# Kernel optimization log

Hardware: AMD Instinct MI355X
Metric: run time of the kernel (lower is better)

The kernel has to match this reference:

```python
import jax, jax.numpy as jnp
import numpy as np

IN_DIM, OUT_DIM, N_PROTO, RANK = 1024, 1024, 32, 16


def setup_inputs() -> dict:
    key = jax.random.key(0)
    ks = jax.random.split(key, 5)
    x = jax.random.normal(ks[0], (2, 4096, IN_DIM), dtype=jnp.float32)
    prototypes = jax.random.normal(ks[1], (N_PROTO, IN_DIM), dtype=jnp.float32) * 0.02
    B = jax.random.normal(ks[2], (N_PROTO, RANK, IN_DIM), dtype=jnp.float32) * 0.02
    A = jax.random.normal(ks[3], (N_PROTO, OUT_DIM, RANK), dtype=jnp.float32) * 0.02
    bias = jnp.zeros((N_PROTO, OUT_DIM), dtype=jnp.float32)
    temp = jnp.asarray(1.0, dtype=jnp.float32)
    return {"x": x, "prototypes": prototypes, "B": B, "A": A, "bias": bias, "temp": temp}


def reference(x, prototypes, B, A, bias, temp):
    lead = x.shape[:-1]
    xf = x.reshape(-1, IN_DIM)                       # [N, in]
    x2 = jnp.sum(xf * xf, axis=1, keepdims=True)     # [N,1]
    p2 = jnp.sum(prototypes * prototypes, axis=1)    # [P]
    d2 = x2 + p2[None, :] - 2.0 * (xf @ prototypes.T)
    dists = jnp.sqrt(jnp.maximum(d2, 0.0))           # [N,P]
    t = jnp.maximum(jnp.abs(temp), 0.1)
    w = jax.nn.softmax(-dists / t, axis=1)           # [N,P]
    topw, topi = jax.lax.top_k(w, 2)                 # [N,2]
    topw = topw / jnp.sum(topw, axis=1, keepdims=True)
    out = jnp.zeros((xf.shape[0], OUT_DIM), dtype=xf.dtype)
    for tslot in range(2):
        idx = topi[:, tslot]                          # [N]
        wt = topw[:, tslot:tslot + 1]                 # [N,1]
        h = jnp.einsum('nri,ni->nr', B[idx], xf)      # gathered low-rank down-proj
        y = jnp.einsum('nor,nr->no', A[idx], h) + bias[idx]
        out = out + wt * y
    return out.reshape(*lead, OUT_DIM)
```

## Files before the change

### kernel.cpp

```cpp
#include <hip/hip_runtime.h>
#include <math.h>

#define ROWS_TOTAL 8192
#define KDIM 1024
#define NPROTO 32
#define RNK 16
#define OUTD 1024
#define TIE_EPS 1.30e-4
#define DELTA 4.0e-5f
#define FLAG_CAP 4096

__global__ __launch_bounds__(256) void prep_kernel(
    const float* __restrict__ A, const float* __restrict__ B,
    const float* __restrict__ proto, float* __restrict__ At,
    float* __restrict__ Bt, float* __restrict__ Pt, double* __restrict__ p2g,
    int* __restrict__ counts, int* __restrict__ flagcnt)
{
    __shared__ float T[16 * 68];
    __shared__ float U[64 * 20];
    __shared__ double red[32][9];
    __shared__ float TP[32][33];
    const int tid = threadIdx.x;

    if (blockIdx.x < 32) {
        const int p = blockIdx.x;
        const float4* B4 = (const float4*)(B + (size_t)p * RNK * KDIM);
        const float4* A4 = (const float4*)(A + (size_t)p * OUTD * RNK);
        float4* Bt4 = (float4*)(Bt + (size_t)p * KDIM * RNK);
        float4* At4 = (float4*)(At + (size_t)p * RNK * OUTD);
        for (int c = 0; c < 16; ++c) {
            {
                int r = tid >> 4, kk = tid & 15;
                float4 v = B4[r * 256 + c * 16 + kk];
                *(float4*)&T[r * 68 + kk * 4] = v;
            }
            {
                int o = tid >> 2, rq = tid & 3;
                float4 v = A4[(c * 64 + o) * 4 + rq];
                *(float4*)&U[o * 20 + rq * 4] = v;
            }
            __syncthreads();
            {
                int k = tid >> 2, rq = tid & 3;
                float4 g = make_float4(T[(rq * 4 + 0) * 68 + k], T[(rq * 4 + 1) * 68 + k],
                                       T[(rq * 4 + 2) * 68 + k], T[(rq * 4 + 3) * 68 + k]);
                Bt4[(c * 64 + k) * 4 + rq] = g;
            }
            {
                int r = tid >> 4, ow = tid & 15;
                float4 g = make_float4(U[(ow * 4 + 0) * 20 + r], U[(ow * 4 + 1) * 20 + r],
                                       U[(ow * 4 + 2) * 20 + r], U[(ow * 4 + 3) * 20 + r]);
                At4[r * 256 + c * 16 + ow] = g;
            }
            __syncthreads();
        }
    } else {
        if (tid < 64) counts[tid] = 0;
        if (tid == 64) flagcnt[0] = 0;
        {
            const int p = tid >> 3, seg = tid & 7;
            const float* a = proto + (size_t)p * KDIM + seg * 128;
            double s = 0.0;
            for (int k = 0; k < 128; ++k) {
                double v = (double)a[k];
                s = fma(v, v, s);
            }
            red[p][seg] = s;
        }
        __syncthreads();
        if (tid < 32) {
            double acc = red[tid][0];
            #pragma unroll
            for (int j = 1; j < 8; ++j) acc += red[tid][j];
            p2g[tid] = acc;
        }
        float4* Pt4 = (float4*)Pt;
        for (int kc = 0; kc < 32; ++kc) {
            {
                int cc = tid >> 3, kk4 = tid & 7;
                float4 v = *(const float4*)(proto + (size_t)cc * KDIM + kc * 32 + kk4 * 4);
                TP[cc][kk4 * 4 + 0] = v.x; TP[cc][kk4 * 4 + 1] = v.y;
                TP[cc][kk4 * 4 + 2] = v.z; TP[cc][kk4 * 4 + 3] = v.w;
            }
            __syncthreads();
            {
                int kk = tid >> 3, c4 = tid & 7;
                float4 g = make_float4(TP[c4 * 4 + 0][kk], TP[c4 * 4 + 1][kk],
                                       TP[c4 * 4 + 2][kk], TP[c4 * 4 + 3][kk]);
                Pt4[(kc * 32 + kk) * 8 + c4] = g;
            }
            __syncthreads();
        }
    }
}

#define INS(kb, ib) { \
    bool lt1 = (kb) < k1, lt2 = (kb) < k2, lt3 = (kb) < k3, lt4 = (kb) < k4; \
    float nk4 = lt3 ? k3 : (lt4 ? (kb) : k4); int ni4 = lt3 ? i3 : (lt4 ? (ib) : i4); \
    float nk3 = lt2 ? k2 : (lt3 ? (kb) : k3); int ni3 = lt2 ? i2 : (lt3 ? (ib) : i3); \
    float nk2 = lt1 ? k1 : (lt2 ? (kb) : k2); int ni2 = lt1 ? i1 : (lt2 ? (ib) : i2); \
    k4 = nk4; i4 = ni4; k3 = nk3; i3 = ni3; k2 = nk2; i2 = ni2; \
    if (lt1) { k1 = (kb); i1 = (ib); } }

__global__ __launch_bounds__(256) void route_kernel(
    const float* __restrict__ x, const float* __restrict__ Pt,
    const float* __restrict__ temp, const double* __restrict__ p2g,
    float4* __restrict__ route, int* __restrict__ counts,
    int* __restrict__ flagcnt, int* __restrict__ flaglist)
{
    __shared__ float Xs[8 * KDIM];
    __shared__ float part[4][8][33];
    __shared__ float x2p[4][8];
    __shared__ int lcnt[64];

    const int tid = threadIdx.x;
    const int w = tid >> 6, l = tid & 63;
    const int c4 = l & 7, kslot = l >> 3;
    const int rowbase = blockIdx.x * 8;

    if (tid < 64) lcnt[tid] = 0;

    const float4* x4 = (const float4*)x;
    float sq[8];
    #pragma unroll
    for (int j = 0; j < 8; ++j) {
        float4 v = x4[(size_t)rowbase * 256 + j * 256 + tid];
        ((float4*)Xs)[j * 256 + tid] = v;
        sq[j] = fmaf(v.x, v.x, fmaf(v.y, v.y, fmaf(v.z, v.z, v.w * v.w)));
    }
    #pragma unroll
    for (int m = 1; m < 64; m <<= 1) {
        #pragma unroll
        for (int j = 0; j < 8; ++j) sq[j] += __shfl_xor(sq[j], m);
    }
    if (l == 0) {
        #pragma unroll
        for (int j = 0; j < 8; ++j) x2p[w][j] = sq[j];
    }
    __syncthreads();

    float acc[8][4];
    #pragma unroll
    for (int j = 0; j < 8; ++j)
        #pragma unroll
        for (int jj = 0; jj < 4; ++jj) acc[j][jj] = 0.f;

    const float4* Pt4 = (const float4*)Pt;
    const int kbase = w * 256;
    #pragma unroll 4
    for (int i = 0; i < 32; ++i) {
        const int k = kbase + i * 8 + kslot;
        float4 pv = Pt4[k * 8 + c4];
        #pragma unroll
        for (int j = 0; j < 8; ++j) {
            float xv = Xs[j * KDIM + k];
            acc[j][0] = fmaf(xv, pv.x, acc[j][0]);
            acc[j][1] = fmaf(xv, pv.y, acc[j][1]);
            acc[j][2] = fmaf(xv, pv.z, acc[j][2]);
            acc[j][3] = fmaf(xv, pv.w, acc[j][3]);
        }
    }
    #pragma unroll
    for (int m = 8; m < 64; m <<= 1) {
        #pragma unroll
        for (int j = 0; j < 8; ++j) {
            acc[j][0] += __shfl_xor(acc[j][0], m);
            acc[j][1] += __shfl_xor(acc[j][1], m);
            acc[j][2] += __shfl_xor(acc[j][2], m);
            acc[j][3] += __shfl_xor(acc[j][3], m);
        }
    }
    if (kslot == 0) {
        #pragma unroll
        for (int j = 0; j < 8; ++j) {
            part[w][j][4 * c4 + 0] = acc[j][0];
            part[w][j][4 * c4 + 1] = acc[j][1];
            part[w][j][4 * c4 + 2] = acc[j][2];
            part[w][j][4 * c4 + 3] = acc[j][3];
        }
    }
    __syncthreads();

    {
        const int rowsel = tid >> 5, c = tid & 31;
        float dsum = (part[0][rowsel][c] + part[1][rowsel][c])
                   + (part[2][rowsel][c] + part[3][rowsel][c]);
        float key = (float)(p2g[c] - 2.0 * (double)dsum);
        float x2 = (x2p[0][rowsel] + x2p[1][rowsel])
                 + (x2p[2][rowsel] + x2p[3][rowsel]);

        float k1 = key, k2 = 3.0e38f, k3 = 3.1e38f, k4 = 3.2e38f;
        int i1 = c, i2 = 64, i3 = 65, i4 = 66;
        #pragma unroll
        for (int m = 1; m < 32; m <<= 1) {
            float b1 = __shfl_xor(k1, m), b2 = __shfl_xor(k2, m);
            float b3 = __shfl_xor(k3, m), b4 = __shfl_xor(k4, m);
            int j1 = __shfl_xor(i1, m), j2 = __shfl_xor(i2, m);
            int j3 = __shfl_xor(i3, m), j4 = __shfl_xor(i4, m);
            INS(b1, j1); INS(b2, j2); INS(b3, j3); INS(b4, j4);
        }
        if (c == 0) {
            const int row = rowbase + rowsel;
            const float tf = fmaxf(fabsf(temp[0]), 0.1f);
            bool amb = (k2 - k1 < DELTA) || (k3 - k2 < DELTA)
                    || (fabsf((k3 - k2) - (float)TIE_EPS) < DELTA)
                    || (k4 - k3 < DELTA);
            bool tie = (k3 - k2) < (float)TIE_EPS;
            bool take3 = tie && (i3 < i2);
            float ksel = take3 ? k3 : k2;
            int   isel = take3 ? i3 : i2;
            float d0 = sqrtf(fmaxf(x2 + k1, 0.f));
            float d1 = sqrtf(fmaxf(x2 + ksel, 0.f));
            float e = expf((d0 - d1) / tf);
            float w0 = 1.f / (1.f + e);
            route[row] = make_float4(__int_as_float(i1), __int_as_float(isel),
                                     w0, e * w0);
            atomicAdd(&lcnt[i1], 1);
            atomicAdd(&lcnt[32 + isel], 1);
            if (amb) {
                int fi = atomicAdd(flagcnt, 1);
                if (fi < FLAG_CAP) flaglist[fi] = row;
            }
        }
    }
    __syncthreads();
    if (tid < 64) atomicAdd(&counts[tid], lcnt[tid]);
}

__global__ __launch_bounds__(256) void refine_scan_kernel(
    const float* __restrict__ x, const float* __restrict__ proto,
    const float* __restrict__ temp, const double* __restrict__ p2g,
    float4* __restrict__ route, int* __restrict__ counts,
    const int* __restrict__ flagcnt, const int* __restrict__ flaglist,
    int2* __restrict__ segs)
{
    const int tid = threadIdx.x;
    const int w = tid >> 6, l = tid & 63;
    const int c = l & 31, half = l >> 5;
    const int n = min(flagcnt[0], FLAG_CAP);

    for (int f = w; f < n; f += 4) {
        const int row = flaglist[f];
        const float* xr = x + (size_t)row * KDIM;
        double xs = 0.0;
        for (int k = l * 16; k < l * 16 + 16; ++k) {
            double v = (double)xr[k];
            xs = fma(v, v, xs);
        }
        #pragma unroll
        for (int m = 1; m < 64; m <<= 1) xs += __shfl_xor(xs, m);
        const float* pr = proto + (size_t)c * KDIM + half * 512;
        const float* xh = xr + half * 512;
        double d0a = 0.0, d1a = 0.0;
        for (int k = 0; k < 512; k += 2) {
            d0a = fma((double)xh[k], (double)pr[k], d0a);
            d1a = fma((double)xh[k + 1], (double)pr[k + 1], d1a);
        }
        double acc = d0a + d1a;
        acc += __shfl_xor(acc, 32);
        double key = p2g[c] - 2.0 * acc;

        double k1 = key, k2 = 1.0e300, k3 = 1.1e300;
        int i1 = c, i2 = 64, i3 = 65;
        #pragma unroll
        for (int m = 1; m < 32; m <<= 1) {
            double b1 = __shfl_xor(k1, m), b2 = __shfl_xor(k2, m), b3 = __shfl_xor(k3, m);
            int j1 = __shfl_xor(i1, m), j2 = __shfl_xor(i2, m), j3 = __shfl_xor(i3, m);
            bool c1 = (k1 < b1) || (k1 == b1 && i1 < j1);
            double m1 = c1 ? k1 : b1, M1 = c1 ? b1 : k1;
            int mi1 = c1 ? i1 : j1, Mi1 = c1 ? j1 : i1;
            bool c2 = (k2 < b2) || (k2 == b2 && i2 < j2);
            double m2 = c2 ? k2 : b2;
            int mi2 = c2 ? i2 : j2;
            bool c3 = (k3 < b3) || (k3 == b3 && i3 < j3);
            double m3 = c3 ? k3 : b3;
            int mi3 = c3 ? i3 : j3;
            bool c4 = (M1 < m2) || (M1 == m2 && Mi1 < mi2);
            double t2 = c4 ? M1 : m2, T2 = c4 ? m2 : M1;
            int ti2 = c4 ? Mi1 : mi2, Ti2 = c4 ? mi2 : Mi1;
            bool c5 = (T2 < m3) || (T2 == m3 && Ti2 < mi3);
            k1 = m1; i1 = mi1;
            k2 = t2; i2 = ti2;
            k3 = c5 ? T2 : m3; i3 = c5 ? Ti2 : mi3;
        }
        if (l == 0) {
            const double tmp = (double)fmaxf(fabsf(temp[0]), 0.1f);
            bool tie = (k3 - k2) < TIE_EPS;
            bool take3 = tie && (i3 < i2);
            double ksel = take3 ? k3 : k2;
            int isel = take3 ? i3 : i2;
            double dd0 = sqrt(fmax(xs + k1, 0.0));
            double dd1 = sqrt(fmax(xs + ksel, 0.0));
            float e = expf((float)((dd0 - dd1) / tmp));
            float w0 = 1.f / (1.f + e);
            float4 old = route[row];
            int oi1 = __float_as_int(old.x), oisel = __float_as_int(old.y);
            if (oi1 != i1) { atomicAdd(&counts[oi1], -1); atomicAdd(&counts[i1], 1); }
            if (oisel != isel) { atomicAdd(&counts[32 + oisel], -1); atomicAdd(&counts[32 + isel], 1); }
            route[row] = make_float4(__int_as_float(i1), __int_as_float(isel),
                                     w0, e * w0);
        }
    }
    __syncthreads();
    if (tid < 64) {
        int v = atomicAdd(&counts[tid], 0);
        int sum = v;
        #pragma unroll
        for (int off = 1; off < 32; off <<= 1) {
            int u = __shfl_up(sum, off, 32);
            if ((tid & 31) >= off) sum += u;
        }
        counts[tid] = sum - v;
        segs[tid] = make_int2(sum - v, sum);
    }
}

__global__ __launch_bounds__(256) void scatter_kernel(
    const float4* __restrict__ route, int* __restrict__ counts,
    int* __restrict__ rowlist0, int* __restrict__ rowlist1)
{
    __shared__ int lcnt[64];
    __shared__ int gbase[64];
    const int tid = threadIdx.x;
    const int i = blockIdx.x * 256 + tid;
    if (tid < 64) lcnt[tid] = 0;
    __syncthreads();
    float4 rt = route[i];
    int p0 = __float_as_int(rt.x);
    int p1 = __float_as_int(rt.y);
    int lp0 = atomicAdd(&lcnt[p0], 1);
    int lp1 = atomicAdd(&lcnt[32 + p1], 1);
    __syncthreads();
    if (tid < 64) gbase[tid] = atomicAdd(&counts[tid], lcnt[tid]);
    __syncthreads();
    rowlist0[gbase[p0] + lp0] = i;
    rowlist1[gbase[32 + p1] + lp1] = i;
}

__global__ __launch_bounds__(256) void h_kernel(
    const float* __restrict__ x, const float* __restrict__ Bt,
    const int* __restrict__ rowlist0, const int* __restrict__ rowlist1,
    const int2* __restrict__ segs, float* __restrict__ hws)
{
    __shared__ float part[4][4][17];
    __shared__ int xoffs[4];

    const int tid = threadIdx.x;
    const int w = tid >> 6, l = tid & 63;
    const int kq = l >> 2, rq = l & 3;
    const int s = blockIdx.y;
    const int slot = s >> 5;
    const int2 sg = segs[s];
    const int* rl = slot ? rowlist1 : rowlist0;
    const float4* Btp = (const float4*)(Bt + (size_t)(s & 31) * KDIM * RNK);
    const int qbase = w * 256;

    for (int c = blockIdx.x; ; c += gridDim.x) {
        const int base = sg.x + c * 4;
        if (base >= sg.y) break;
        const int m = min(4, sg.y - base);

        if (tid < 4) xoffs[tid] = rl[base + min(tid, m - 1)] * KDIM;
        __syncthreads();
        const int x0 = xoffs[0], x1 = xoffs[1], x2 = xoffs[2], x3 = xoffs[3];

        float4 a0 = {0,0,0,0}, a1 = {0,0,0,0}, a2 = {0,0,0,0}, a3 = {0,0,0,0};
        #pragma unroll
        for (int i = 0; i < 16; ++i) {
            const int k = qbase + i * 16 + kq;
            float4 bv = Btp[k * 4 + rq];
            float v0 = x[x0 + k], v1 = x[x1 + k], v2 = x[x2 + k], v3 = x[x3 + k];
            a0.x = fmaf(v0, bv.x, a0.x); a0.y = fmaf(v0, bv.y, a0.y);
            a0.z = fmaf(v0, bv.z, a0.z); a0.w = fmaf(v0, bv.w, a0.w);
            a1.x = fmaf(v1, bv.x, a1.x); a1.y = fmaf(v1, bv.y, a1.y);
            a1.z = fmaf(v1, bv.z, a1.z); a1.w = fmaf(v1, bv.w, a1.w);
            a2.x = fmaf(v2, bv.x, a2.x); a2.y = fmaf(v2, bv.y, a2.y);
            a2.z = fmaf(v2, bv.z, a2.z); a2.w = fmaf(v2, bv.w, a2.w);
            a3.x = fmaf(v3, bv.x, a3.x); a3.y = fmaf(v3, bv.y, a3.y);
            a3.z = fmaf(v3, bv.z, a3.z); a3.w = fmaf(v3, bv.w, a3.w);
        }
        #pragma unroll
        for (int msk = 4; msk < 64; msk <<= 1) {
            a0.x += __shfl_xor(a0.x, msk); a0.y += __shfl_xor(a0.y, msk);
            a0.z += __shfl_xor(a0.z, msk); a0.w += __shfl_xor(a0.w, msk);
            a1.x += __shfl_xor(a1.x, msk); a1.y += __shfl_xor(a1.y, msk);
            a1.z += __shfl_xor(a1.z, msk); a1.w += __shfl_xor(a1.w, msk);
            a2.x += __shfl_xor(a2.x, msk); a2.y += __shfl_xor(a2.y, msk);
            a2.z += __shfl_xor(a2.z, msk); a2.w += __shfl_xor(a2.w, msk);
            a3.x += __shfl_xor(a3.x, msk); a3.y += __shfl_xor(a3.y, msk);
            a3.z += __shfl_xor(a3.z, msk); a3.w += __shfl_xor(a3.w, msk);
        }
        if (kq == 0) {
            *(float4*)&part[w][0][rq * 4] = a0;
            *(float4*)&part[w][1][rq * 4] = a1;
            *(float4*)&part[w][2][rq * 4] = a2;
            *(float4*)&part[w][3][rq * 4] = a3;
        }
        __syncthreads();
        if (tid < 64) {
            const int e = tid >> 4, r = tid & 15;
            if (e < m) {
                float hsum = part[0][e][r] + part[1][e][r]
                           + part[2][e][r] + part[3][e][r];
                hws[(size_t)(slot * ROWS_TOTAL + base + e) * 16 + r] = hsum;
            }
        }
        __syncthreads();
    }
}

__global__ __launch_bounds__(256) void y_kernel(
    const float* __restrict__ At, const float* __restrict__ bias,
    const float4* __restrict__ route, const int* __restrict__ rowlist,
    const int2* __restrict__ segs, const float* __restrict__ hws,
    float* __restrict__ out, int slot)
{
    __shared__ float hsm[16][17];
    __shared__ int rows[16];
    __shared__ float wts[16];

    const int tid = threadIdx.x;
    const int f4 = tid;
    const int p = blockIdx.y;
    const int2 sg = segs[slot * 32 + p];
    const float4* Atp = (const float4*)(At + (size_t)p * RNK * OUTD);
    const float4 bb = ((const float4*)(bias + (size_t)p * OUTD))[f4];

    float4 Areg[16];
    #pragma unroll
    for (int r = 0; r < 16; ++r) Areg[r] = Atp[r * 256 + f4];

    for (int c = blockIdx.x; ; c += gridDim.x) {
        const int base = sg.x + c * 16;
        if (base >= sg.y) break;
        const int m = min(16, sg.y - base);
        const int gbase = slot * ROWS_TOTAL + base;

        if (tid < 16) {
            int rr = rowlist[base + min(tid, m - 1)];
            rows[tid] = rr;
            float4 rt = route[rr];
            wts[tid] = slot ? rt.w : rt.z;
        }
        {
            const int e = tid >> 4, r = tid & 15;
            hsm[e][r] = hws[(size_t)(gbase + min(e, m - 1)) * 16 + r];
        }
        __syncthreads();

        for (int e = 0; e < m; ++e) {
            float4 acc = bb;
            #pragma unroll
            for (int r = 0; r < 16; ++r) {
                float hr = hsm[e][r];
                acc.x = fmaf(hr, Areg[r].x, acc.x);
                acc.y = fmaf(hr, Areg[r].y, acc.y);
                acc.z = fmaf(hr, Areg[r].z, acc.z);
                acc.w = fmaf(hr, Areg[r].w, acc.w);
            }
            const float w = wts[e];
            float4 v = make_float4(w * acc.x, w * acc.y, w * acc.z, w * acc.w);
            float4* dst = (float4*)(out + (size_t)rows[e] * OUTD) + f4;
            if (slot) {
                float4 old = *dst;
                v.x += old.x; v.y += old.y; v.z += old.z; v.w += old.w;
            }
            *dst = v;
        }
        __syncthreads();
    }
}

extern "C" void kernel_launch(void* const* d_in, const int* in_sizes, int n_in,
                              void* d_out, int out_size, void* d_ws, size_t ws_size,
                              hipStream_t stream) {
    const float* x     = (const float*)d_in[0];
    const float* proto = (const float*)d_in[1];
    const float* B     = (const float*)d_in[2];
    const float* A     = (const float*)d_in[3];
    const float* bias  = (const float*)d_in[4];
    const float* temp  = (const float*)d_in[5];
    float* out = (float*)d_out;

    char* wsb = (char*)d_ws;
    float4* route = (float4*)wsb;
    int* rowlist0 = (int*)(wsb + 131072);
    int* rowlist1 = rowlist0 + ROWS_TOTAL;
    int* counts   = (int*)(wsb + 196608);
    int2* segs    = (int2*)(wsb + 196864);
    double* p2g   = (double*)(wsb + 197376);
    int* flagcnt  = (int*)(wsb + 197632);
    int* flaglist = (int*)(wsb + 197760);
    float* Pt     = (float*)(wsb + 262144);
    float* Bt     = (float*)(wsb + 393216);
    float* At     = (float*)(wsb + 393216 + 2097152);
    float* hws    = (float*)(wsb + 393216 + 2 * 2097152);

    prep_kernel<<<33, 256, 0, stream>>>(A, B, proto, At, Bt, Pt, p2g,
                                        counts, flagcnt);
    route_kernel<<<ROWS_TOTAL / 8, 256, 0, stream>>>(x, Pt, temp, p2g, route,
                                                     counts, flagcnt, flaglist);
    refine_scan_kernel<<<1, 256, 0, stream>>>(x, proto, temp, p2g, route,
                                              counts, flagcnt, flaglist, segs);
    scatter_kernel<<<ROWS_TOTAL / 256, 256, 0, stream>>>(route, counts, rowlist0, rowlist1);
    h_kernel<<<dim3(64, 64), 256, 0, stream>>>(x, Bt, rowlist0, rowlist1, segs, hws);
    y_kernel<<<dim3(16, NPROTO), 256, 0, stream>>>(At, bias, route, rowlist0, segs, hws, out, 0);
    y_kernel<<<dim3(16, NPROTO), 256, 0, stream>>>(At, bias, route, rowlist1, segs, hws, out, 1);
}
```

Before: 158.2 us.

## Use single-wave blocks in h_kernel to drop shared-memory cross-wave reduction

h_kernel now runs one 64-thread wavefront per block. Each wave covers the whole K dimension (64 iterations) instead of four waves splitting K, so the shared-memory partial sums and all __syncthreads barriers go away. Row offsets are read directly by every lane, and results are written straight to global memory with float4 stores. The trade-off is four times less parallelism per row group and longer serial loops, which may hurt latency hiding since the grid size is unchanged.

```diff
diff --git a/kernel.cpp b/kernel.cpp
--- a/kernel.cpp
+++ b/kernel.cpp
@@ -337,37 +337,33 @@
     rowlist1[gbase[32 + p1] + lp1] = i;
 }
 
-__global__ __launch_bounds__(256) void h_kernel(
+__global__ __launch_bounds__(64) void h_kernel(
     const float* __restrict__ x, const float* __restrict__ Bt,
     const int* __restrict__ rowlist0, const int* __restrict__ rowlist1,
     const int2* __restrict__ segs, float* __restrict__ hws)
 {
-    __shared__ float part[4][4][17];
-    __shared__ int xoffs[4];
-
-    const int tid = threadIdx.x;
-    const int w = tid >> 6, l = tid & 63;
+    const int l = threadIdx.x;
     const int kq = l >> 2, rq = l & 3;
     const int s = blockIdx.y;
     const int slot = s >> 5;
     const int2 sg = segs[s];
     const int* rl = slot ? rowlist1 : rowlist0;
     const float4* Btp = (const float4*)(Bt + (size_t)(s & 31) * KDIM * RNK);
-    const int qbase = w * 256;
-
-    for (int c = blockIdx.x; ; c += gridDim.x) {
+
+    for (int c = blockIdx.x; ; c += 64) {
         const int base = sg.x + c * 4;
         if (base >= sg.y) break;
         const int m = min(4, sg.y - base);
 
-        if (tid < 4) xoffs[tid] = rl[base + min(tid, m - 1)] * KDIM;
-        __syncthreads();
-        const int x0 = xoffs[0], x1 = xoffs[1], x2 = xoffs[2], x3 = xoffs[3];
+        const int x0 = rl[base + 0] * KDIM;
+        const int x1 = rl[base + min(1, m - 1)] * KDIM;
+        const int x2 = rl[base + min(2, m - 1)] * KDIM;
+        const int x3 = rl[base + min(3, m - 1)] * KDIM;
 
         float4 a0 = {0,0,0,0}, a1 = {0,0,0,0}, a2 = {0,0,0,0}, a3 = {0,0,0,0};
-        #pragma unroll
-        for (int i = 0; i < 16; ++i) {
-            const int k = qbase + i * 16 + kq;
+        #pragma unroll 8
+        for (int i = 0; i < 64; ++i) {
+            const int k = i * 16 + kq;
             float4 bv = Btp[k * 4 + rq];
             float v0 = x[x0 + k], v1 = x[x1 + k], v2 = x[x2 + k], v3 = x[x3 + k];
             a0.x = fmaf(v0, bv.x, a0.x); a0.y = fmaf(v0, bv.y, a0.y);
@@ -391,21 +387,12 @@
             a3.z += __shfl_xor(a3.z, msk); a3.w += __shfl_xor(a3.w, msk);
         }
         if (kq == 0) {
-            *(float4*)&part[w][0][rq * 4] = a0;
-            *(float4*)&part[w][1][rq * 4] = a1;
-            *(float4*)&part[w][2][rq * 4] = a2;
-            *(float4*)&part[w][3][rq * 4] = a3;
-        }
-        __syncthreads();
-        if (tid < 64) {
-            const int e = tid >> 4, r = tid & 15;
-            if (e < m) {
-                float hsum = part[0][e][r] + part[1][e][r]
-                           + part[2][e][r] + part[3][e][r];
-                hws[(size_t)(slot * ROWS_TOTAL + base + e) * 16 + r] = hsum;
-            }
-        }
-        __syncthreads();
+            const size_t gb = (size_t)(slot * ROWS_TOTAL + base);
+            *(float4*)(hws + (gb + 0) * 16 + rq * 4) = a0;
+            if (m > 1) *(float4*)(hws + (gb + 1) * 16 + rq * 4) = a1;
+            if (m > 2) *(float4*)(hws + (gb + 2) * 16 + rq * 4) = a2;
+            if (m > 3) *(float4*)(hws + (gb + 3) * 16 + rq * 4) = a3;
+        }
     }
 }
 
@@ -503,7 +490,7 @@
     refine_scan_kernel<<<1, 256, 0, stream>>>(x, proto, temp, p2g, route,
                                               counts, flagcnt, flaglist, segs);
     scatter_kernel<<<ROWS_TOTAL / 256, 256, 0, stream>>>(route, counts, rowlist0, rowlist1);
-    h_kernel<<<dim3(64, 64), 256, 0, stream>>>(x, Bt, rowlist0, rowlist1, segs, hws);
+    h_kernel<<<dim3(64, 64), 64, 0, stream>>>(x, Bt, rowlist0, rowlist1, segs, hws);
     y_kernel<<<dim3(16, NPROTO), 256, 0, stream>>>(At, bias, route, rowlist0, segs, hws, out, 0);
     y_kernel<<<dim3(16, NPROTO), 256, 0, stream>>>(At, bias, route, rowlist1, segs, hws, out, 1);
 }
```

After: 178.8 us. +13.1%, slower.
